# Optimization experiments

Hardware: AMD Instinct MI355X
Metric: run time of the kernel (lower is better)

Reference implementation:

```python
import jax, jax.numpy as jnp
import numpy as np


def _to_complex(e):
    # e: [..., L, 2] (real, imag) -> complex64 [..., L]
    return e[..., 0] + 1j * e[..., 1]


def _idct_last(x, expk):
    # IDCT (DCT-III-like, no normalization, full weight on x_0) along last axis:
    #   y_u = sum_{k=0}^{N-1} x_k cos(pi*k*(2u+1)/(2N))
    # Makhoul FFT algorithm: t = N*ifft(x * exp(i*pi*k/(2N)));
    #   y_{2n} = Re t_n, y_{2n+1} = Re t_{N-1-n}
    N = x.shape[-1]
    t = jnp.fft.ifft(x * expk, axis=-1) * N
    re = jnp.real(t).astype(x.dtype)
    y = jnp.zeros_like(x)
    y = y.at[..., 0::2].set(re[..., : (N + 1) // 2])
    y = y.at[..., 1::2].set(re[..., ::-1][..., : N // 2])
    return y


def _idxst_last(x, expk):
    # IDXST along last axis: y_u = sum_{k=0}^{N-1} x_k sin(pi*k*(2u+1)/(2N))
    # Identity: sin(pi*k*(2u+1)/(2N)) = (-1)^u cos(pi*(N-k)*(2u+1)/(2N))
    # => y = (-1)^u * idct(x') with x'_0 = 0, x'_j = x_{N-j}
    N = x.shape[-1]
    xp = jnp.concatenate([jnp.zeros_like(x[..., :1]), x[..., :0:-1]], axis=-1)
    sign = jnp.where(jnp.arange(N) % 2 == 0, 1.0, -1.0).astype(x.dtype)
    return _idct_last(xp, expk) * sign


def setup_inputs() -> dict:
    key = jax.random.key(0)
    M, N = 4096, 4096
    x = jax.random.normal(key, (M, N), dtype=jnp.float32)
    kM = np.arange(M)
    kN = np.arange(N)
    expkM = np.stack([np.cos(np.pi * kM / (2 * M)), np.sin(np.pi * kM / (2 * M))], axis=-1).astype(np.float32)
    expkN = np.stack([np.cos(np.pi * kN / (2 * N)), np.sin(np.pi * kN / (2 * N))], axis=-1).astype(np.float32)
    return {"x": x, "expkM": jnp.asarray(expkM), "expkN": jnp.asarray(expkN)}


def reference(x, expkM, expkN):
    # 2D separable transform: IDXST along dim 0 (M), IDCT along dim 1 (N)
    eM = _to_complex(expkM)
    eN = _to_complex(expkN)
    y = _idxst_last(x.T, eM).T  # idxst over rows (size M)
    y = _idct_last(y, eN)       # idct over cols (size N)
    return y
```

## Files before the change

kernel.cpp:

```cpp
#include <hip/hip_runtime.h>
#include <hip/hip_bf16.h>

typedef __bf16 bf16x8 __attribute__((ext_vector_type(8)));
typedef float  f32x4  __attribute__((ext_vector_type(4)));

__device__ __forceinline__ unsigned short f2bf(float f) {
    union { float f; unsigned int u; } v; v.f = f;
    unsigned int r = v.u + 0x7FFFu + ((v.u >> 16) & 1u);
    return (unsigned short)(r >> 16);
}

__device__ __forceinline__ void async16(const unsigned short* g, unsigned short* l) {
    __builtin_amdgcn_global_load_lds(
        (const __attribute__((address_space(1))) unsigned int*)g,
        (__attribute__((address_space(3))) unsigned int*)l,
        16, 0, 0);
}

__global__ __launch_bounds__(256) void transpose_perm(
    const float* __restrict__ X, unsigned short* __restrict__ Xt, int Mr, int Nc)
{
    __shared__ float tile[64][65];
    const int bx = blockIdx.x * 64;
    const int by = blockIdx.y * 64;
    const int tid = threadIdx.x;
    const int halfM = Mr >> 1;

    const int c4 = (tid & 15) * 4;
    const int r  = tid >> 4;
#pragma unroll
    for (int p = 0; p < 4; ++p) {
        const float4 v = *reinterpret_cast<const float4*>(
            &X[(size_t)(by + r + 16 * p) * Nc + bx + c4]);
        tile[r + 16 * p][c4 + 0] = v.x;
        tile[r + 16 * p][c4 + 1] = v.y;
        tile[r + 16 * p][c4 + 2] = v.z;
        tile[r + 16 * p][c4 + 3] = v.w;
    }
    __syncthreads();

    const int q  = tid & 7;
    const int h  = (tid >> 3) & 1;
    const int n0 = tid >> 4;
#pragma unroll
    for (int p = 0; p < 4; ++p) {
        const int n = n0 + 16 * p;
        ushort4 o;
        o.x = f2bf(tile[8 * q + 0 + h][n]);
        o.y = f2bf(tile[8 * q + 2 + h][n]);
        o.z = f2bf(tile[8 * q + 4 + h][n]);
        o.w = f2bf(tile[8 * q + 6 + h][n]);
        *reinterpret_cast<ushort4*>(
            Xt + (size_t)(bx + n) * Mr + h * halfM + (by >> 1) + 4 * q) = o;
    }
}

__global__ __launch_bounds__(256) void gen_w(
    unsigned short* __restrict__ out, int doSin)
{
    const int flat = (int)(((size_t)blockIdx.x * 256 + threadIdx.x) * 4);
    const int r  = flat >> 12;
    const int c0 = flat & 4095;
    const unsigned int step = 2u * (unsigned int)r + 1u;
    const float scale = 3.14159265358979323846f / 8192.0f;
    unsigned short o[4];
#pragma unroll
    for (int j = 0; j < 4; ++j) {
        const int c = c0 + j;
        const unsigned int kk = (c < 2048) ? (unsigned int)(2 * c)
                                           : (unsigned int)(2 * (c - 2048) + 1);
        unsigned int p = (kk * step) & 16383u;
        float ang = (float)p * scale;
        float v = doSin ? __sinf(ang) : __cosf(ang);
        o[j] = f2bf(v);
    }
    uint2 pack;
    pack.x = (unsigned int)o[0] | ((unsigned int)o[1] << 16);
    pack.y = (unsigned int)o[2] | ((unsigned int)o[3] << 16);
    *reinterpret_cast<uint2*>(out + flat) = pack;
}

#define BARRIER __builtin_amdgcn_s_barrier()
#define LGKM0 asm volatile("s_waitcnt lgkmcnt(0)" ::: "memory")
#define VM0 asm volatile("s_waitcnt vmcnt(0)" ::: "memory")
#define PRIO1 __builtin_amdgcn_s_setprio(1)
#define PRIO0 __builtin_amdgcn_s_setprio(0)

#define STAGE(LB, KC) do { \
    _Pragma("unroll") for (int p = 0; p < 8; ++p) \
        async16(srcp_[p] + (KC), &lds[(LB) + ((p * 256 + wbase) * 8)]); } while (0)

#define LD_ALL(LB) do { \
    _Pragma("unroll") for (int mm = 0; mm < 4; ++mm) { \
        af[mm][0] = *(const bf16x8*)&lds[(LB) + aOff + mm * 1024 + sl0]; \
        af[mm][1] = *(const bf16x8*)&lds[(LB) + aOff + mm * 1024 + sl1]; } \
    _Pragma("unroll") for (int nn = 0; nn < 4; ++nn) { \
        bfr[nn][0] = *(const bf16x8*)&lds[(LB) + bOff + nn * 1024 + sl0]; \
        bfr[nn][1] = *(const bf16x8*)&lds[(LB) + bOff + nn * 1024 + sl1]; } } while (0)

#define MFMA_ALL(ACC) do { \
    _Pragma("unroll") for (int ks = 0; ks < 2; ++ks) \
    _Pragma("unroll") for (int mm = 0; mm < 4; ++mm) \
    _Pragma("unroll") for (int nn = 0; nn < 4; ++nn) \
        ACC[mm][nn] = __builtin_amdgcn_mfma_f32_16x16x32_bf16( \
            af[mm][ks], bfr[nn][ks], ACC[mm][nn], 0, 0, 0); } while (0)

template <int EPI, typename OutT>
__global__ __launch_bounds__(256, 2) void gemm_fused(
    const unsigned short* __restrict__ P,
    const unsigned short* __restrict__ Q,
    OutT* __restrict__ C, int nbx)
{
    __shared__ __align__(16) unsigned short lds[2 * 4 * 4096];

    const int tid  = threadIdx.x;
    const int lane = tid & 63;
    const int w    = tid >> 6;
    const int wm   = w >> 1;
    const int wn   = w & 1;

    const int bid = blockIdx.x;
    const int wg  = (bid & 7) * (gridDim.x >> 3) + (bid >> 3);
    const int brow = (wg / nbx) * 128;
    const int bcol = (wg % nbx) * 128;

    const unsigned short* srcp_[8];
    const int wbase = tid & ~63;
#pragma unroll
    for (int p = 0; p < 8; ++p) {
        const int c    = p * 256 + tid;
        const int unit = c >> 9;
        const int urow = (c >> 3) & 63;
        const int slot = c & 7;
        const int sx   = (slot ^ (urow & 7)) << 3;
        srcp_[p] = (unit < 2)
            ? P + (size_t)(brow + unit * 64 + urow) * 4096 + sx
            : Q + (size_t)(bcol + (unit - 2) * 64 + urow) * 4096 + sx;
    }

    const int lr = lane & 15, lk = lane >> 4, sx = lr & 7;
    const int sl0 = ((lk) ^ sx) << 3;
    const int sl1 = ((4 + lk) ^ sx) << 3;
    const int aOff = wm * 4096 + lr * 64;
    const int bOff = (2 + wn) * 4096 + lr * 64;

    bf16x8 af[4][2], bfr[4][2];
    f32x4 accE[4][4] = {};
    f32x4 accO[4][4] = {};

    STAGE(0, 0);
    VM0;
    BARRIER;

    for (int t = 0; t < 32; ++t) {
        const int lb = (t & 1) << 14;
        const int nb = lb ^ 16384;
        STAGE(nb, (t + 1) << 6);
        LD_ALL(lb);
        PRIO1; MFMA_ALL(accE); PRIO0;
        LGKM0; VM0; BARRIER;
    }
    for (int t = 32; t < 63; ++t) {
        const int lb = (t & 1) << 14;
        const int nb = lb ^ 16384;
        STAGE(nb, (t + 1) << 6);
        LD_ALL(lb);
        PRIO1; MFMA_ALL(accO); PRIO0;
        LGKM0; VM0; BARRIER;
    }
    {
        const int lb = (63 & 1) << 14;
        LD_ALL(lb);
        PRIO1; MFMA_ALL(accO); PRIO0;
    }

    const int r0 = brow + wm * 64 + (lane >> 4) * 4;
    const int c0 = bcol + wn * 64 + (lane & 15);
#pragma unroll
    for (int mf = 0; mf < 4; ++mf)
#pragma unroll
        for (int nf = 0; nf < 4; ++nf)
#pragma unroll
            for (int r = 0; r < 4; ++r) {
                const int row = r0 + mf * 16 + r;
                const int col = c0 + nf * 16;
                const float e = accE[mf][nf][r];
                const float o = accO[mf][nf][r];
                if (EPI == 1) {
                    const int pin = (col >> 1) + ((col & 1) << 11);
                    ((unsigned short*)C)[(size_t)row * 4096 + pin] = f2bf(e + o);
                    ((unsigned short*)C)[(size_t)(4095 - row) * 4096 + pin] = f2bf(o - e);
                } else {
                    ((float*)C)[(size_t)row * 4096 + col] = e + o;
                    ((float*)C)[(size_t)row * 4096 + 4095 - col] = e - o;
                }
            }
}

extern "C" void kernel_launch(void* const* d_in, const int* in_sizes, int n_in,
                              void* d_out, int out_size, void* d_ws, size_t ws_size,
                              hipStream_t stream) {
    const float* X = (const float*)d_in[0];
    const int Mr = in_sizes[1] / 2;
    const int Nc = in_sizes[2] / 2;

    unsigned short* R0 = (unsigned short*)d_ws;
    unsigned short* R1 = R0 + (size_t)Mr * Nc;
    unsigned short* R2 = R1 + (size_t)(Mr / 2) * Nc;

    transpose_perm<<<dim3(Nc / 64, Mr / 64), 256, 0, stream>>>(X, R0, Mr, Nc);
    gen_w<<<(2048 * 4096 / 4) / 256, 256, 0, stream>>>(R1, 1);
    gemm_fused<1, unsigned short><<<512, 256, 0, stream>>>(R1, R0, R2, 32);
    gen_w<<<(2048 * 4096 / 4) / 256, 256, 0, stream>>>(R1, 0);
    gemm_fused<2, float><<<512, 256, 0, stream>>>(R2, R1, (float*)d_out, 16);
}
```

Before: 168.2 us.

## Apply a second level of even/odd butterfly decomposition to the DCT GEMMs

```diff
diff --git a/kernel.cpp b/kernel.cpp
--- a/kernel.cpp
+++ b/kernel.cpp
@@ -8,6 +8,9 @@
     union { float f; unsigned int u; } v; v.f = f;
     unsigned int r = v.u + 0x7FFFu + ((v.u >> 16) & 1u);
     return (unsigned short)(r >> 16);
+}
+__device__ __forceinline__ float bf2f(unsigned short h) {
+    union { unsigned int u; float f; } v; v.u = ((unsigned int)h) << 16; return v.f;
 }
 
 __device__ __forceinline__ void async16(const unsigned short* g, unsigned short* l) {
@@ -17,21 +20,20 @@
         16, 0, 0);
 }
 
-__global__ __launch_bounds__(256) void transpose_perm(
-    const float* __restrict__ X, unsigned short* __restrict__ Xt, int Mr, int Nc)
+__global__ __launch_bounds__(256) void transpose_perm4(
+    const float* __restrict__ X, unsigned short* __restrict__ Xt)
 {
     __shared__ float tile[64][65];
     const int bx = blockIdx.x * 64;
     const int by = blockIdx.y * 64;
     const int tid = threadIdx.x;
-    const int halfM = Mr >> 1;
 
     const int c4 = (tid & 15) * 4;
     const int r  = tid >> 4;
 #pragma unroll
     for (int p = 0; p < 4; ++p) {
         const float4 v = *reinterpret_cast<const float4*>(
-            &X[(size_t)(by + r + 16 * p) * Nc + bx + c4]);
+            &X[(size_t)(by + r + 16 * p) * 4096 + bx + c4]);
         tile[r + 16 * p][c4 + 0] = v.x;
         tile[r + 16 * p][c4 + 1] = v.y;
         tile[r + 16 * p][c4 + 2] = v.z;
@@ -39,40 +41,77 @@
     }
     __syncthreads();
 
-    const int q  = tid & 7;
-    const int h  = (tid >> 3) & 1;
+    const int g  = tid & 15;
     const int n0 = tid >> 4;
 #pragma unroll
     for (int p = 0; p < 4; ++p) {
         const int n = n0 + 16 * p;
+        unsigned short* row = Xt + (size_t)(bx + n) * 4096;
         ushort4 o;
-        o.x = f2bf(tile[8 * q + 0 + h][n]);
-        o.y = f2bf(tile[8 * q + 2 + h][n]);
-        o.z = f2bf(tile[8 * q + 4 + h][n]);
-        o.w = f2bf(tile[8 * q + 6 + h][n]);
-        *reinterpret_cast<ushort4*>(
-            Xt + (size_t)(bx + n) * Mr + h * halfM + (by >> 1) + 4 * q) = o;
-    }
-}
-
-__global__ __launch_bounds__(256) void gen_w(
+        if (g < 4) {
+            o.x = f2bf(tile[16 * g + 0][n]);
+            o.y = f2bf(tile[16 * g + 4][n]);
+            o.z = f2bf(tile[16 * g + 8][n]);
+            o.w = f2bf(tile[16 * g + 12][n]);
+            *reinterpret_cast<ushort4*>(row + (by >> 2) + 4 * g) = o;
+        } else if (g < 8) {
+            const int g2 = g - 4;
+            o.x = f2bf(tile[16 * g2 + 2][n]);
+            o.y = f2bf(tile[16 * g2 + 6][n]);
+            o.z = f2bf(tile[16 * g2 + 10][n]);
+            o.w = f2bf(tile[16 * g2 + 14][n]);
+            *reinterpret_cast<ushort4*>(row + 1024 + (by >> 2) + 4 * g2) = o;
+        } else {
+            const int g3 = g - 8;
+            o.x = f2bf(tile[8 * g3 + 1][n]);
+            o.y = f2bf(tile[8 * g3 + 3][n]);
+            o.z = f2bf(tile[8 * g3 + 5][n]);
+            o.w = f2bf(tile[8 * g3 + 7][n]);
+            *reinterpret_cast<ushort4*>(row + 2048 + (by >> 1) + 4 * g3) = o;
+        }
+    }
+}
+
+__global__ __launch_bounds__(256) void gen_w12(
     unsigned short* __restrict__ out, int doSin)
 {
     const int flat = (int)(((size_t)blockIdx.x * 256 + threadIdx.x) * 4);
-    const int r  = flat >> 12;
-    const int c0 = flat & 4095;
-    const unsigned int step = 2u * (unsigned int)r + 1u;
-    const float scale = 3.14159265358979323846f / 8192.0f;
+    const int u  = flat >> 11;
+    const int c0 = flat & 2047;
+    const unsigned int step = 2u * (unsigned int)u + 1u;
     unsigned short o[4];
 #pragma unroll
     for (int j = 0; j < 4; ++j) {
         const int c = c0 + j;
-        const unsigned int kk = (c < 2048) ? (unsigned int)(2 * c)
-                                           : (unsigned int)(2 * (c - 2048) + 1);
-        unsigned int p = (kk * step) & 16383u;
-        float ang = (float)p * scale;
-        float v = doSin ? __sinf(ang) : __cosf(ang);
-        o[j] = f2bf(v);
+        float ang;
+        if (c < 1024) {
+            unsigned int p = ((unsigned int)c * step) & 4095u;
+            ang = (float)p * (3.14159265358979323846f / 2048.0f);
+        } else {
+            unsigned int p = ((unsigned int)(2 * (c - 1024) + 1) * step) & 8191u;
+            ang = (float)p * (3.14159265358979323846f / 4096.0f);
+        }
+        o[j] = f2bf(doSin ? __sinf(ang) : __cosf(ang));
+    }
+    uint2 pack;
+    pack.x = (unsigned int)o[0] | ((unsigned int)o[1] << 16);
+    pack.y = (unsigned int)o[2] | ((unsigned int)o[3] << 16);
+    *reinterpret_cast<uint2*>(out + flat) = pack;
+}
+
+__global__ __launch_bounds__(256) void gen_wO(
+    unsigned short* __restrict__ out, int doSin)
+{
+    const int flat = (int)(((size_t)blockIdx.x * 256 + threadIdx.x) * 4);
+    const int u  = flat >> 11;
+    const int c0 = flat & 2047;
+    const unsigned int step = 2u * (unsigned int)u + 1u;
+    unsigned short o[4];
+#pragma unroll
+    for (int j = 0; j < 4; ++j) {
+        unsigned int p = ((unsigned int)(2 * (c0 + j) + 1) * step) & 16383u;
+        float ang = (float)p * (3.14159265358979323846f / 8192.0f);
+        o[j] = f2bf(doSin ? __sinf(ang) : __cosf(ang));
     }
     uint2 pack;
     pack.x = (unsigned int)o[0] | ((unsigned int)o[1] << 16);
@@ -86,11 +125,119 @@
 #define PRIO1 __builtin_amdgcn_s_setprio(1)
 #define PRIO0 __builtin_amdgcn_s_setprio(0)
 
-#define STAGE(LB, KC) do { \
+#define S_STAGE(LB, KC) do { \
+    _Pragma("unroll") for (int p = 0; p < 6; ++p) \
+        async16(srcp_[p] + (KC), &lds[(LB) + ((p * 256 + wbase) * 8)]); } while (0)
+
+#define S_LD(LB) do { \
+    _Pragma("unroll") for (int mm = 0; mm < 4; ++mm) { \
+        af[mm][0] = *(const bf16x8*)&lds[(LB) + aOff + mm * 1024 + sl0]; \
+        af[mm][1] = *(const bf16x8*)&lds[(LB) + aOff + mm * 1024 + sl1]; } \
+    _Pragma("unroll") for (int nn = 0; nn < 2; ++nn) { \
+        bfr[nn][0] = *(const bf16x8*)&lds[(LB) + bOff + nn * 1024 + sl0]; \
+        bfr[nn][1] = *(const bf16x8*)&lds[(LB) + bOff + nn * 1024 + sl1]; } } while (0)
+
+#define S_MFMA(ACC) do { \
+    _Pragma("unroll") for (int ks = 0; ks < 2; ++ks) \
+    _Pragma("unroll") for (int mm = 0; mm < 4; ++mm) \
+    _Pragma("unroll") for (int nn = 0; nn < 2; ++nn) \
+        ACC[mm][nn] = __builtin_amdgcn_mfma_f32_16x16x32_bf16( \
+            af[mm][ks], bfr[nn][ks], ACC[mm][nn], 0, 0, 0); } while (0)
+
+template <int EPI>
+__global__ __launch_bounds__(256, 2) void gemm_small(
+    const unsigned short* __restrict__ P,
+    const unsigned short* __restrict__ Q,
+    unsigned short* __restrict__ E,
+    int ldp, int ldq, int nbx)
+{
+    __shared__ __align__(16) unsigned short lds[2 * 3 * 4096];
+
+    const int tid  = threadIdx.x;
+    const int lane = tid & 63;
+    const int w    = tid >> 6;
+    const int wm   = w >> 1;
+    const int wn   = w & 1;
+
+    const int bid = blockIdx.x;
+    const int wg  = (bid & 7) * (gridDim.x >> 3) + (bid >> 3);
+    const int brow = (wg / nbx) * 128;
+    const int bcol = (wg % nbx) * 64;
+
+    const unsigned short* srcp_[6];
+    const int wbase = tid & ~63;
+#pragma unroll
+    for (int p = 0; p < 6; ++p) {
+        const int c    = p * 256 + tid;
+        const int unit = c >> 9;
+        const int urow = (c >> 3) & 63;
+        const int slot = c & 7;
+        const int sx   = (slot ^ (urow & 7)) << 3;
+        srcp_[p] = (unit < 2)
+            ? P + (size_t)(brow + unit * 64 + urow) * ldp + sx
+            : Q + (size_t)(bcol + urow) * ldq + sx;
+    }
+
+    const int lr = lane & 15, lk = lane >> 4, sx = lr & 7;
+    const int sl0 = ((lk) ^ sx) << 3;
+    const int sl1 = ((4 + lk) ^ sx) << 3;
+    const int aOff = wm * 4096 + lr * 64;
+    const int bOff = 2 * 4096 + wn * 2048 + lr * 64;
+
+    bf16x8 af[4][2], bfr[2][2];
+    f32x4 aE[4][2] = {};
+    f32x4 aO[4][2] = {};
+
+    S_STAGE(0, 0);
+    VM0;
+    BARRIER;
+
+    for (int t = 0; t < 16; ++t) {
+        const int lb = (t & 1) ? 12288 : 0;
+        S_STAGE(lb ^ 12288, (t + 1) << 6);
+        S_LD(lb);
+        PRIO1; S_MFMA(aE); PRIO0;
+        LGKM0; VM0; BARRIER;
+    }
+    for (int t = 16; t < 31; ++t) {
+        const int lb = (t & 1) ? 12288 : 0;
+        S_STAGE(lb ^ 12288, (t + 1) << 6);
+        S_LD(lb);
+        PRIO1; S_MFMA(aO); PRIO0;
+        LGKM0; VM0; BARRIER;
+    }
+    {
+        S_LD(12288);
+        PRIO1; S_MFMA(aO); PRIO0;
+    }
+
+    const int r0 = brow + wm * 64 + (lane >> 4) * 4;
+    const int c0 = bcol + wn * 32 + (lane & 15);
+#pragma unroll
+    for (int mf = 0; mf < 4; ++mf)
+#pragma unroll
+        for (int nf = 0; nf < 2; ++nf)
+#pragma unroll
+            for (int r = 0; r < 4; ++r) {
+                const int i = r0 + mf * 16 + r;
+                const int j = c0 + nf * 16;
+                const float e2 = aE[mf][nf][r];
+                const float o2 = aO[mf][nf][r];
+                if (EPI == 1) {
+                    E[(size_t)i * 4096 + j] = f2bf(e2 + o2);
+                    E[(size_t)(2047 - i) * 4096 + j] = f2bf(o2 - e2);
+                } else {
+                    E[(size_t)i * 2048 + j] = f2bf(e2 + o2);
+                    E[(size_t)i * 2048 + 2047 - j] = f2bf(e2 - o2);
+                }
+            }
+}
+
+#define B_STAGE(LB, KC) do { \
     _Pragma("unroll") for (int p = 0; p < 8; ++p) \
         async16(srcp_[p] + (KC), &lds[(LB) + ((p * 256 + wbase) * 8)]); } while (0)
 
-#define LD_ALL(LB) do { \
+#define B_LD(LB) do { \
     _Pragma("unroll") for (int mm = 0; mm < 4; ++mm) { \
         af[mm][0] = *(const bf16x8*)&lds[(LB) + aOff + mm * 1024 + sl0]; \
         af[mm][1] = *(const bf16x8*)&lds[(LB) + aOff + mm * 1024 + sl1]; } \
@@ -98,7 +245,7 @@
         bfr[nn][0] = *(const bf16x8*)&lds[(LB) + bOff + nn * 1024 + sl0]; \
         bfr[nn][1] = *(const bf16x8*)&lds[(LB) + bOff + nn * 1024 + sl1]; } } while (0)
 
-#define MFMA_ALL(ACC) do { \
+#define B_MFMA(ACC) do { \
     _Pragma("unroll") for (int ks = 0; ks < 2; ++ks) \
     _Pragma("unroll") for (int mm = 0; mm < 4; ++mm) \
     _Pragma("unroll") for (int nn = 0; nn < 4; ++nn) \
@@ -106,10 +253,12 @@
             af[mm][ks], bfr[nn][ks], ACC[mm][nn], 0, 0, 0); } while (0)
 
 template <int EPI, typename OutT>
-__global__ __launch_bounds__(256, 2) void gemm_fused(
+__global__ __launch_bounds__(256, 2) void gemm_big(
     const unsigned short* __restrict__ P,
     const unsigned short* __restrict__ Q,
-    OutT* __restrict__ C, int nbx)
+    OutT* __restrict__ C,
+    const unsigned short* __restrict__ E,
+    int ldp, int ldq, int nbx)
 {
     __shared__ __align__(16) unsigned short lds[2 * 4 * 4096];
 
@@ -134,8 +283,8 @@
         const int slot = c & 7;
         const int sx   = (slot ^ (urow & 7)) << 3;
         srcp_[p] = (unit < 2)
-            ? P + (size_t)(brow + unit * 64 + urow) * 4096 + sx
-            : Q + (size_t)(bcol + (unit - 2) * 64 + urow) * 4096 + sx;
+            ? P + (size_t)(brow + unit * 64 + urow) * ldp + sx
+            : Q + (size_t)(bcol + (unit - 2) * 64 + urow) * ldq + sx;
     }
 
     const int lr = lane & 15, lk = lane >> 4, sx = lr & 7;
@@ -145,33 +294,22 @@
     const int bOff = (2 + wn) * 4096 + lr * 64;
 
     bf16x8 af[4][2], bfr[4][2];
-    f32x4 accE[4][4] = {};
-    f32x4 accO[4][4] = {};
-
-    STAGE(0, 0);
+    f32x4 acc[4][4] = {};
+
+    B_STAGE(0, 0);
     VM0;
     BARRIER;
 
-    for (int t = 0; t < 32; ++t) {
+    for (int t = 0; t < 31; ++t) {
         const int lb = (t & 1) << 14;
-        const int nb = lb ^ 16384;
-        STAGE(nb, (t + 1) << 6);
-        LD_ALL(lb);
-        PRIO1; MFMA_ALL(accE); PRIO0;
+        B_STAGE(lb ^ 16384, (t + 1) << 6);
+        B_LD(lb);
+        PRIO1; B_MFMA(acc); PRIO0;
         LGKM0; VM0; BARRIER;
     }
-    for (int t = 32; t < 63; ++t) {
-        const int lb = (t & 1) << 14;
-        const int nb = lb ^ 16384;
-        STAGE(nb, (t + 1) << 6);
-        LD_ALL(lb);
-        PRIO1; MFMA_ALL(accO); PRIO0;
-        LGKM0; VM0; BARRIER;
-    }
     {
-        const int lb = (63 & 1) << 14;
-        LD_ALL(lb);
-        PRIO1; MFMA_ALL(accO); PRIO0;
+        B_LD(16384);
+        PRIO1; B_MFMA(acc); PRIO0;
     }
 
     const int r0 = brow + wm * 64 + (lane >> 4) * 4;
@@ -182,17 +320,19 @@
         for (int nf = 0; nf < 4; ++nf)
 #pragma unroll
             for (int r = 0; r < 4; ++r) {
-                const int row = r0 + mf * 16 + r;
-                const int col = c0 + nf * 16;
-                const float e = accE[mf][nf][r];
-                const float o = accO[mf][nf][r];
+                const int i = r0 + mf * 16 + r;
+                const int j = c0 + nf * 16;
+                const float o = acc[mf][nf][r];
                 if (EPI == 1) {
-                    const int pin = (col >> 1) + ((col & 1) << 11);
-                    ((unsigned short*)C)[(size_t)row * 4096 + pin] = f2bf(e + o);
-                    ((unsigned short*)C)[(size_t)(4095 - row) * 4096 + pin] = f2bf(o - e);
+                    const float e = bf2f(E[(size_t)i * 4096 + j]);
+                    const int pin = (j & 1) ? 2048 + (j >> 1)
+                                  : ((j & 2) ? 1024 + (j >> 2) : (j >> 2));
+                    ((unsigned short*)C)[(size_t)i * 4096 + pin] = f2bf(e + o);
+                    ((unsigned short*)C)[(size_t)(4095 - i) * 4096 + pin] = f2bf(o - e);
                 } else {
-                    ((float*)C)[(size_t)row * 4096 + col] = e + o;
-                    ((float*)C)[(size_t)row * 4096 + 4095 - col] = e - o;
+                    const float e = bf2f(E[(size_t)i * 2048 + j]);
+                    ((float*)C)[(size_t)i * 4096 + j] = e + o;
+                    ((float*)C)[(size_t)i * 4096 + 4095 - j] = e - o;
                 }
             }
 }
@@ -201,16 +341,22 @@
                               void* d_out, int out_size, void* d_ws, size_t ws_size,
                               hipStream_t stream) {
     const float* X = (const float*)d_in[0];
-    const int Mr = in_sizes[1] / 2;
-    const int Nc = in_sizes[2] / 2;
-
-    unsigned short* R0 = (unsigned short*)d_ws;
-    unsigned short* R1 = R0 + (size_t)Mr * Nc;
-    unsigned short* R2 = R1 + (size_t)(Mr / 2) * Nc;
-
-    transpose_perm<<<dim3(Nc / 64, Mr / 64), 256, 0, stream>>>(X, R0, Mr, Nc);
-    gen_w<<<(2048 * 4096 / 4) / 256, 256, 0, stream>>>(R1, 1);
-    gemm_fused<1, unsigned short><<<512, 256, 0, stream>>>(R1, R0, R2, 32);
-    gen_w<<<(2048 * 4096 / 4) / 256, 256, 0, stream>>>(R1, 0);
-    gemm_fused<2, float><<<512, 256, 0, stream>>>(R2, R1, (float*)d_out, 16);
-}
+
+    unsigned short* Xt  = (unsigned short*)d_ws;
+    unsigned short* T   = Xt + (size_t)4096 * 4096;
+    unsigned short* E   = T + (size_t)4096 * 4096;
+    unsigned short* W12 = E + (size_t)2048 * 4096;
+    unsigned short* WO  = W12 + (size_t)1024 * 2048;
+
+    transpose_perm4<<<dim3(64, 64), 256, 0, stream>>>(X, Xt);
+
+    gen_w12<<<2048, 256, 0, stream>>>(W12, 1);
+    gen_wO<<<4096, 256, 0, stream>>>(WO, 1);
+    gemm_small<1><<<512, 256, 0, stream>>>(W12, Xt, E, 2048, 4096, 64);
+    gemm_big<1, unsigned short><<<512, 256, 0, stream>>>(WO, Xt + 2048, T, E, 2048, 4096, 32);
+
+    gen_w12<<<2048, 256, 0, stream>>>(W12, 0);
+    gen_wO<<<4096, 256, 0, stream>>>(WO, 0);
+    gemm_small<2><<<512, 256, 0, stream>>>(T, W12, E, 4096, 2048, 16);
+    gemm_big<2, float><<<512, 256, 0, stream>>>(T + 2048, WO, (float*)d_out, E, 4096, 2048, 16);
+}
```

New measurement: 181.3 us. 1.08x slower.

## Load A operand directly from global into registers, stage only B in LDS

Applied to the files above, without the earlier changes.

```diff
diff --git a/kernel.cpp b/kernel.cpp
--- a/kernel.cpp
+++ b/kernel.cpp
@@ -86,14 +86,16 @@
 #define PRIO1 __builtin_amdgcn_s_setprio(1)
 #define PRIO0 __builtin_amdgcn_s_setprio(0)
 
-#define STAGE(LB, KC) do { \
-    _Pragma("unroll") for (int p = 0; p < 8; ++p) \
+#define STAGE_B(LB, KC) do { \
+    _Pragma("unroll") for (int p = 0; p < 4; ++p) \
         async16(srcp_[p] + (KC), &lds[(LB) + ((p * 256 + wbase) * 8)]); } while (0)
 
-#define LD_ALL(LB) do { \
+#define LOADA(KC) do { \
     _Pragma("unroll") for (int mm = 0; mm < 4; ++mm) { \
-        af[mm][0] = *(const bf16x8*)&lds[(LB) + aOff + mm * 1024 + sl0]; \
-        af[mm][1] = *(const bf16x8*)&lds[(LB) + aOff + mm * 1024 + sl1]; } \
+        af[mm][0] = *(const bf16x8*)(pa_[mm] + (KC)); \
+        af[mm][1] = *(const bf16x8*)(pa_[mm] + (KC) + 32); } } while (0)
+
+#define LD_B(LB) do { \
     _Pragma("unroll") for (int nn = 0; nn < 4; ++nn) { \
         bfr[nn][0] = *(const bf16x8*)&lds[(LB) + bOff + nn * 1024 + sl0]; \
         bfr[nn][1] = *(const bf16x8*)&lds[(LB) + bOff + nn * 1024 + sl1]; } } while (0)
@@ -111,7 +113,7 @@
     const unsigned short* __restrict__ Q,
     OutT* __restrict__ C, int nbx)
 {
-    __shared__ __align__(16) unsigned short lds[2 * 4 * 4096];
+    __shared__ __align__(16) unsigned short lds[2 * 2 * 4096];
 
     const int tid  = threadIdx.x;
     const int lane = tid & 63;
@@ -124,53 +126,56 @@
     const int brow = (wg / nbx) * 128;
     const int bcol = (wg % nbx) * 128;
 
-    const unsigned short* srcp_[8];
+    const unsigned short* srcp_[4];
     const int wbase = tid & ~63;
 #pragma unroll
-    for (int p = 0; p < 8; ++p) {
+    for (int p = 0; p < 4; ++p) {
         const int c    = p * 256 + tid;
         const int unit = c >> 9;
         const int urow = (c >> 3) & 63;
         const int slot = c & 7;
         const int sx   = (slot ^ (urow & 7)) << 3;
-        srcp_[p] = (unit < 2)
-            ? P + (size_t)(brow + unit * 64 + urow) * 4096 + sx
-            : Q + (size_t)(bcol + (unit - 2) * 64 + urow) * 4096 + sx;
-    }
+        srcp_[p] = Q + (size_t)(bcol + unit * 64 + urow) * 4096 + sx;
+    }
+
+    const unsigned short* pa_[4];
+    const int arow = brow + wm * 64 + (lane & 15);
+#pragma unroll
+    for (int mm = 0; mm < 4; ++mm)
+        pa_[mm] = P + (size_t)(arow + mm * 16) * 4096 + (lane >> 4) * 8;
 
     const int lr = lane & 15, lk = lane >> 4, sx = lr & 7;
     const int sl0 = ((lk) ^ sx) << 3;
     const int sl1 = ((4 + lk) ^ sx) << 3;
-    const int aOff = wm * 4096 + lr * 64;
-    const int bOff = (2 + wn) * 4096 + lr * 64;
+    const int bOff = wn * 4096 + lr * 64;
 
     bf16x8 af[4][2], bfr[4][2];
     f32x4 accE[4][4] = {};
     f32x4 accO[4][4] = {};
 
-    STAGE(0, 0);
+    STAGE_B(0, 0);
     VM0;
     BARRIER;
 
     for (int t = 0; t < 32; ++t) {
-        const int lb = (t & 1) << 14;
-        const int nb = lb ^ 16384;
-        STAGE(nb, (t + 1) << 6);
-        LD_ALL(lb);
+        const int lb = (t & 1) << 13;
+        LOADA(t << 6);
+        STAGE_B(lb ^ 8192, (t + 1) << 6);
+        LD_B(lb);
         PRIO1; MFMA_ALL(accE); PRIO0;
         LGKM0; VM0; BARRIER;
     }
     for (int t = 32; t < 63; ++t) {
-        const int lb = (t & 1) << 14;
-        const int nb = lb ^ 16384;
-        STAGE(nb, (t + 1) << 6);
-        LD_ALL(lb);
+        const int lb = (t & 1) << 13;
+        LOADA(t << 6);
+        STAGE_B(lb ^ 8192, (t + 1) << 6);
+        LD_B(lb);
         PRIO1; MFMA_ALL(accO); PRIO0;
         LGKM0; VM0; BARRIER;
     }
     {
-        const int lb = (63 & 1) << 14;
-        LD_ALL(lb);
+        LOADA(63 << 6);
+        LD_B(8192);
         PRIO1; MFMA_ALL(accO); PRIO0;
     }
 
```

New measurement: 311.1 us. 1.85x slower.

## Single-buffer GEMM LDS staging and raise occupancy hint to four blocks

Applied to the files above, without the earlier changes.

```diff
diff --git a/kernel.cpp b/kernel.cpp
--- a/kernel.cpp
+++ b/kernel.cpp
@@ -86,17 +86,17 @@
 #define PRIO1 __builtin_amdgcn_s_setprio(1)
 #define PRIO0 __builtin_amdgcn_s_setprio(0)
 
-#define STAGE(LB, KC) do { \
+#define STAGE(KC) do { \
     _Pragma("unroll") for (int p = 0; p < 8; ++p) \
-        async16(srcp_[p] + (KC), &lds[(LB) + ((p * 256 + wbase) * 8)]); } while (0)
-
-#define LD_ALL(LB) do { \
+        async16(srcp_[p] + (KC), &lds[((p * 256 + wbase) * 8)]); } while (0)
+
+#define LD_ALL() do { \
     _Pragma("unroll") for (int mm = 0; mm < 4; ++mm) { \
-        af[mm][0] = *(const bf16x8*)&lds[(LB) + aOff + mm * 1024 + sl0]; \
-        af[mm][1] = *(const bf16x8*)&lds[(LB) + aOff + mm * 1024 + sl1]; } \
+        af[mm][0] = *(const bf16x8*)&lds[aOff + mm * 1024 + sl0]; \
+        af[mm][1] = *(const bf16x8*)&lds[aOff + mm * 1024 + sl1]; } \
     _Pragma("unroll") for (int nn = 0; nn < 4; ++nn) { \
-        bfr[nn][0] = *(const bf16x8*)&lds[(LB) + bOff + nn * 1024 + sl0]; \
-        bfr[nn][1] = *(const bf16x8*)&lds[(LB) + bOff + nn * 1024 + sl1]; } } while (0)
+        bfr[nn][0] = *(const bf16x8*)&lds[bOff + nn * 1024 + sl0]; \
+        bfr[nn][1] = *(const bf16x8*)&lds[bOff + nn * 1024 + sl1]; } } while (0)
 
 #define MFMA_ALL(ACC) do { \
     _Pragma("unroll") for (int ks = 0; ks < 2; ++ks) \
@@ -106,12 +106,12 @@
             af[mm][ks], bfr[nn][ks], ACC[mm][nn], 0, 0, 0); } while (0)
 
 template <int EPI, typename OutT>
-__global__ __launch_bounds__(256, 2) void gemm_fused(
+__global__ __launch_bounds__(256, 4) void gemm_fused(
     const unsigned short* __restrict__ P,
     const unsigned short* __restrict__ Q,
     OutT* __restrict__ C, int nbx)
 {
-    __shared__ __align__(16) unsigned short lds[2 * 4 * 4096];
+    __shared__ __align__(16) unsigned short lds[4 * 4096];
 
     const int tid  = threadIdx.x;
     const int lane = tid & 63;
@@ -148,29 +148,29 @@
     f32x4 accE[4][4] = {};
     f32x4 accO[4][4] = {};
 
-    STAGE(0, 0);
+    STAGE(0);
     VM0;
     BARRIER;
 
     for (int t = 0; t < 32; ++t) {
-        const int lb = (t & 1) << 14;
-        const int nb = lb ^ 16384;
-        STAGE(nb, (t + 1) << 6);
-        LD_ALL(lb);
+        LD_ALL();
+        LGKM0;
+        BARRIER;
+        STAGE((t + 1) << 6);
         PRIO1; MFMA_ALL(accE); PRIO0;
-        LGKM0; VM0; BARRIER;
+        VM0; BARRIER;
     }
     for (int t = 32; t < 63; ++t) {
-        const int lb = (t & 1) << 14;
-        const int nb = lb ^ 16384;
-        STAGE(nb, (t + 1) << 6);
-        LD_ALL(lb);
+        LD_ALL();
+        LGKM0;
+        BARRIER;
+        STAGE((t + 1) << 6);
         PRIO1; MFMA_ALL(accO); PRIO0;
-        LGKM0; VM0; BARRIER;
+        VM0; BARRIER;
     }
     {
-        const int lb = (63 & 1) << 14;
-        LD_ALL(lb);
+        LD_ALL();
+        LGKM0;
         PRIO1; MFMA_ALL(accO); PRIO0;
     }
 
```

Result: slower. 649.2 us (+286.0%).
